# Kernel optimization log

Measured on AMD Instinct MI355X. Metric: run time of the kernel, lower is better.

Reference implementation:

```python
import jax, jax.numpy as jnp
import numpy as np

DIM = 256
HEADS = 8
DIM_HEAD = 32
INNER = HEADS * DIM_HEAD  # 256
SCALE = DIM_HEAD ** -0.5
NEG = -100.0

MASK0 = jnp.array([[0., 0., 0., NEG],
                   [0., 0., NEG, 0.],
                   [0., NEG, 0., 0.],
                   [NEG, 0., 0., 0.]], dtype=jnp.float32)
MASK1 = jnp.array([[0., NEG, 0., NEG],
                   [NEG, 0., NEG, 0.],
                   [NEG, NEG, NEG, NEG],
                   [NEG, NEG, NEG, NEG]], dtype=jnp.float32)


def setup_inputs() -> dict:
    key = jax.random.key(0)
    ks = jax.random.split(key, 8)
    b, p, d = 8, 3136, DIM
    return {
        "x": jax.random.normal(ks[0], (b, p, d), jnp.float32),
        "y": jax.random.normal(ks[1], (b, p, d), jnp.float32),
        "Wqkv_z": jax.random.normal(ks[2], (3 * INNER, d), jnp.float32) * 0.02,
        "Wout_z": jax.random.normal(ks[3], (d, INNER), jnp.float32) * 0.02,
        "bout_z": jnp.zeros((d,), jnp.float32),
        "Wqkv_z1": jax.random.normal(ks[4], (3 * INNER, d), jnp.float32) * 0.02,
        "Wout_z1": jax.random.normal(ks[5], (d, INNER), jnp.float32) * 0.02,
        "bout_z1": jnp.zeros((d,), jnp.float32),
    }


def _attn_stage(z, Wqkv, Wout, bout, mask):
    # z: [b, p, n=4, d]
    b, p, n, d = z.shape
    qkv = jnp.einsum('bpnd,ed->bpne', z, Wqkv)  # [b,p,4,3*inner]
    q, k, v = jnp.split(qkv, 3, axis=-1)
    def heads(t):  # [b,p,n,inner] -> [b,p,h,n,dh]
        return t.reshape(b, p, n, HEADS, DIM_HEAD).transpose(0, 1, 3, 2, 4)
    q, k, v = heads(q), heads(k), heads(v)
    dots = jnp.einsum('bphid,bphjd->bphij', q, k) * SCALE + mask
    attn = jax.nn.softmax(dots, axis=-1)
    out = jnp.einsum('bphij,bphjd->bphid', attn, v)
    out = out.transpose(0, 1, 3, 2, 4).reshape(b, p, n, INNER)
    return jnp.einsum('bpne,de->bpnd', out, Wout) + bout


def reference(x, y, Wqkv_z, Wout_z, bout_z, Wqkv_z1, Wout_z1, bout_z1):
    b, p, d = x.shape
    rgb_g = jnp.mean(x, axis=1, keepdims=True)    # avg_pool1d over p == mean
    dep_g = jnp.mean(y, axis=1, keepdims=True)
    rgb_g = jnp.broadcast_to(rgb_g, (b, p, d))
    dep_g = jnp.broadcast_to(dep_g, (b, p, d))
    z = jnp.stack([x, y, rgb_g, dep_g], axis=2)   # [b,p,4,d]
    z_out = _attn_stage(z, Wqkv_z, Wout_z, bout_z, MASK0)
    z_out1 = _attn_stage(z_out, Wqkv_z1, Wout_z1, bout_z1, MASK1)
    x1 = z_out1[:, :, 0, :]
    y1 = z_out1[:, :, 1, :]
    return (x1, y1)
```

## Files before the change

### kernel.cpp

```cpp
#include <hip/hip_runtime.h>

typedef unsigned short u16;
typedef unsigned int   u32;
typedef short bf16x8 __attribute__((ext_vector_type(8)));
typedef float f32x16 __attribute__((ext_vector_type(16)));

#define NB    8
#define NP    3136
#define DIM   256
#define PTILE 16
#define NEGM  (-100.0f)
#define QKSCALE 0.17677669529663687f

#define LDS_SZ  65536
#define Q0B     16384
#define K0B     32768
#define P0B     49152
#define Q1B     49152
#define P1B     32768
#define AO1LB   16384

__device__ __forceinline__ float bflo(u32 w) { return __uint_as_float(w << 16); }
__device__ __forceinline__ float bfhi(u32 w) { return __uint_as_float(w & 0xffff0000u); }

__device__ __forceinline__ u32 cvt_pk(float a, float b) {
  u32 r;
  asm("v_cvt_pk_bf16_f32 %0, %1, %2" : "=v"(r) : "v"(a), "v"(b));
  return r;
}

__device__ __forceinline__ void phase_fence() { __builtin_amdgcn_sched_barrier(0); }

template<int MASKI>
__device__ __forceinline__ float maskv(int i, int j) {
  if (MASKI == 0) return ((i ^ j) == 3) ? NEGM : 0.f;
  return (i >= 2 || ((i ^ j) & 1)) ? NEGM : 0.f;
}

#define FRAG(nt, ks) ((((size_t)(nt) * 16 + (ks)) * 64 + lane) * 8)

__device__ __forceinline__ void pack4(const float* __restrict__ W,
                                      u16* __restrict__ hi, u16* __restrict__ lo,
                                      int is_qkv, int pair0, int tid) {
  const int p    = pair0 + (tid >> 6);
  const int lane = tid & 63;
  const int nt = p >> 4, ks = p & 15;
  const int n  = nt * 32 + (lane & 31);
  const int k0 = ks * 16 + ((lane >> 5) << 3);
  const float scale = (is_qkv && n < 256) ? QKSCALE : 1.0f;
  const float* src = W + (size_t)n * 256 + k0;
  const size_t o = (((size_t)nt * 16 + ks) * 64 + lane) * 8;
#pragma unroll
  for (int j = 0; j < 8; j++) {
    float v = src[j] * scale;
    u32 wh = cvt_pk(v, v);
    hi[o + j] = (u16)wh;
    if (lo) lo[o + j] = (u16)cvt_pk(v - bflo(wh), 0.f);
  }
}

__global__ __launch_bounds__(256)
void prep1(const float* __restrict__ x, const float* __restrict__ y,
           float* __restrict__ part,
           const float* __restrict__ wqkv0, u16* __restrict__ wq0_hi,
           const float* __restrict__ wout1, u16* __restrict__ wo1_hi, u16* __restrict__ wo1_lo,
           const float* __restrict__ wqkv1, const float* __restrict__ wout0,
           float* __restrict__ Wc,
           const float* __restrict__ bout0, float* __restrict__ bq) {
  __shared__ float srow[256];
  const int bid = blockIdx.x;
  const int tid = threadIdx.x;
  if (bid < 1568) {
    const int ab = bid / 98;
    const int chunk = bid - ab * 98;
    const int b = ab & 7;
    const float* src = (ab >> 3) ? y : x;
    float s = 0.f;
    const int p0 = chunk * 32;
#pragma unroll 4
    for (int i = 0; i < 32; i++)
      s += src[((size_t)b * NP + p0 + i) * DIM + tid];
    part[((size_t)ab * 98 + chunk) * DIM + tid] = s;
  } else if (bid < 1664) {
    pack4(wqkv0, wq0_hi, nullptr, 1, (bid - 1568) * 4, tid);
  } else if (bid < 1696) {
    pack4(wout1, wo1_hi, wo1_lo, 0, (bid - 1664) * 4, tid);
  } else if (bid < 2464) {
    const int n = bid - 1696;
    srow[tid] = wqkv1[(size_t)n * 256 + tid];
    __syncthreads();
    float acc = 0.f;
#pragma unroll 8
    for (int d = 0; d < 256; d++)
      acc += srow[d] * wout0[(size_t)d * 256 + tid];
    Wc[(size_t)n * 256 + tid] = acc;
  } else {
    const int n = (bid - 2464) * 256 + tid;
    float s = 0.f;
    for (int d = 0; d < 256; d += 4) {
      const float4 w = *(const float4*)(wqkv1 + (size_t)n * 256 + d);
      const float4 bv = *(const float4*)(bout0 + d);
      s += w.x * bv.x + w.y * bv.y + w.z * bv.z + w.w * bv.w;
    }
    bq[n] = (n < 256) ? s * QKSCALE : s;
  }
}

__global__ __launch_bounds__(256)
void prep2(const float* __restrict__ part, const float* __restrict__ wqkv0,
           float* __restrict__ qkvg,
           const float* __restrict__ Wc, u16* __restrict__ wc_hi, u16* __restrict__ wc_lo) {
  __shared__ float srow[256];
  const int bid = blockIdx.x;
  const int tid = threadIdx.x;
  if (bid < 16) {
    float s = 0.f;
    for (int c = 0; c < 98; c++) s += part[((size_t)bid * 98 + c) * DIM + tid];
    srow[tid] = s * (1.0f / 3136.0f);
    __syncthreads();
    const int bt = (bid < 8) ? (2 * bid) : (2 * (bid - 8) + 1);
#pragma unroll
    for (int sct = 0; sct < 3; sct++) {
      const int e = sct * 256 + tid;
      float acc = 0.f;
      for (int d = 0; d < 256; d += 4) {
        const float4 w = *(const float4*)(wqkv0 + (size_t)e * 256 + d);
        acc += w.x * srow[d] + w.y * srow[d + 1] + w.z * srow[d + 2] + w.w * srow[d + 3];
      }
      qkvg[(size_t)bt * 768 + e] = (e < 256) ? acc * QKSCALE : acc;
    }
  } else {
    pack4(Wc, wc_hi, wc_lo, 1, (bid - 16) * 4, tid);
  }
}

__global__ __launch_bounds__(512, 4)
void fused_kernel(const float* __restrict__ x, const float* __restrict__ y,
                  const float* __restrict__ qkvg, float* __restrict__ outp,
                  const u16* __restrict__ wq0_hi,
                  const u16* __restrict__ wc_hi,  const u16* __restrict__ wc_lo,
                  const u16* __restrict__ wo1_hi, const u16* __restrict__ wo1_lo,
                  const float* __restrict__ bq,   const float* __restrict__ bout1) {
  extern __shared__ char lds[];
  const int tid  = threadIdx.x;
  const int lane = tid & 63;
  const int wave = tid >> 6;
  const int cl   = lane & 31;
  const int rh5  = lane >> 5;
  const int kgrp = rh5 << 3;
  const int b    = blockIdx.y;
  const int pos0 = blockIdx.x * PTILE;
  const int apos = wave * 2 + rh5;
  const int ah   = (lane >> 2) & 7;
  const int adq  = lane & 3;
  const float* qg = qkvg + (size_t)(b * 2) * 768;

  {
    const int r   = tid >> 4;
    const int cb  = (tid & 15) * 16;
    const int pos = pos0 + (r >> 1);
    const float* src = ((r & 1) ? y : x) + ((size_t)b * NP + pos) * DIM;
#pragma unroll
    for (int u = 0; u < 4; u++) {
      const int col = cb + u * 4;
      float4 v = *(const float4*)(src + col);
      uint2 hw;
      hw.x = cvt_pk(v.x, v.y);
      hw.y = cvt_pk(v.z, v.w);
      *(uint2*)(lds + ((r * 512 + col * 2) ^ ((r & 15) << 4))) = hw;
    }
  }
  __syncthreads();
  phase_fence();

  f32x16 av;
  {
    f32x16 aq, ak;
#pragma unroll
    for (int i = 0; i < 16; i++) { aq[i] = 0.f; ak[i] = 0.f; av[i] = 0.f; }
#pragma unroll 2
    for (int ks = 0; ks < 16; ks++) {
      const int k0 = ks * 16 + kgrp;
      bf16x8 ahf = *(const bf16x8*)(lds + ((cl * 512 + k0 * 2) ^ ((cl & 15) << 4)));
      bf16x8 bQ = *(const bf16x8*)(wq0_hi + FRAG(wave, ks));
      bf16x8 bK = *(const bf16x8*)(wq0_hi + FRAG(8 + wave, ks));
      bf16x8 bV = *(const bf16x8*)(wq0_hi + FRAG(16 + wave, ks));
      __builtin_amdgcn_s_setprio(1);
      aq = __builtin_amdgcn_mfma_f32_32x32x16_bf16(ahf, bQ, aq, 0, 0, 0);
      ak = __builtin_amdgcn_mfma_f32_32x32x16_bf16(ahf, bK, ak, 0, 0, 0);
      av = __builtin_amdgcn_mfma_f32_32x32x16_bf16(ahf, bV, av, 0, 0, 0);
      __builtin_amdgcn_s_setprio(0);
    }
    const int sw0 = ((cl ^ wave) & 7) << 3;
    const int bQd = Q0B + wave * 2048 + cl * 64;
    const int bKd = K0B + wave * 2048 + cl * 64;
#pragma unroll
    for (int gq = 0; gq < 4; gq++) {
      const int p20 = 8 * gq + 4 * rh5;
      uint2 wv;
      wv.x = cvt_pk(aq[4 * gq + 0], aq[4 * gq + 1]);
      wv.y = cvt_pk(aq[4 * gq + 2], aq[4 * gq + 3]);
      *(uint2*)(lds + bQd + ((p20 * 2) ^ sw0)) = wv;
      wv.x = cvt_pk(ak[4 * gq + 0], ak[4 * gq + 1]);
      wv.y = cvt_pk(ak[4 * gq + 2], ak[4 * gq + 3]);
      *(uint2*)(lds + bKd + ((p20 * 2) ^ sw0)) = wv;
    }
  }
  __syncthreads();
  phase_fence();

  {
    const int e0 = ah * 32 + adq * 8;
    float dots[4][4];
#pragma unroll
    for (int i = 0; i < 4; i++)
#pragma unroll
      for (int j = 0; j < 4; j++) dots[i][j] = 0.f;
#pragma unroll 2
    for (int dd = 0; dd < 8; dd++) {
      const int d = adq * 8 + dd;
      const int sw = ((d ^ ah) & 7) << 3;
      u32 qw = *(const u32*)(lds + Q0B + ah * 2048 + d * 64 + ((apos * 4) ^ sw));
      u32 kw = *(const u32*)(lds + K0B + ah * 2048 + d * 64 + ((apos * 4) ^ sw));
      float q[4] = { bflo(qw), bfhi(qw), qg[e0 + dd], qg[768 + e0 + dd] };
      float k[4] = { bflo(kw), bfhi(kw), qg[256 + e0 + dd], qg[1024 + e0 + dd] };
#pragma unroll
      for (int i = 0; i < 4; i++)
#pragma unroll
        for (int j = 0; j < 4; j++) dots[i][j] += q[i] * k[j];
    }
#pragma unroll
    for (int i = 0; i < 4; i++)
#pragma unroll
      for (int j = 0; j < 4; j++) {
        float s = dots[i][j];
        s += __shfl_xor(s, 1);
        s += __shfl_xor(s, 2);
        dots[i][j] = s + maskv<0>(i, j);
      }
    if (adq == 0) {
#pragma unroll
      for (int i = 0; i < 4; i++) {
        const float mx = fmaxf(fmaxf(dots[i][0], dots[i][1]), fmaxf(dots[i][2], dots[i][3]));
        const float e0_ = __expf(dots[i][0] - mx), e1_ = __expf(dots[i][1] - mx);
        const float e2_ = __expf(dots[i][2] - mx), e3_ = __expf(dots[i][3] - mx);
        const float inv = 1.f / (e0_ + e1_ + e2_ + e3_);
        float4 pv_ = { e0_ * inv, e1_ * inv, e2_ * inv, e3_ * inv };
        *(float4*)(lds + P0B + ((apos * 8 + ah) * 4 + i) * 16) = pv_;
      }
    }
  }
  __syncthreads();
  phase_fence();

  {
    const float vg2 = qg[512 + wave * 32 + cl];
    const float vg3 = qg[768 + 512 + wave * 32 + cl];
    const int c = wave * 32 + cl;
#pragma unroll
    for (int gq = 0; gq < 4; gq++) {
#pragma unroll
      for (int pp = 0; pp < 2; pp++) {
        const int pos = 4 * gq + 2 * rh5 + pp;
        const float v0 = av[4 * gq + 2 * pp], v1 = av[4 * gq + 2 * pp + 1];
#pragma unroll
        for (int i = 0; i < 4; i++) {
          float4 pi = *(const float4*)(lds + P0B + ((pos * 8 + wave) * 4 + i) * 16);
          const float o = pi.x * v0 + pi.y * v1 + pi.z * vg2 + pi.w * vg3;
          const int R = pos * 4 + i;
          *(u16*)(lds + ((R * 512 + c * 2) ^ ((R & 15) << 4))) = (u16)cvt_pk(o, o);
        }
      }
    }
  }
  __syncthreads();
  phase_fence();

  {
    f32x16 aq0, aq1;
#pragma unroll
    for (int i = 0; i < 16; i++) { aq0[i] = 0.f; aq1[i] = 0.f; }
#pragma unroll 1
    for (int ks = 0; ks < 16; ks++) {
      const int k0 = ks * 16 + kgrp;
      bf16x8 ah0 = *(const bf16x8*)(lds + ((cl * 512 + k0 * 2) ^ ((cl & 15) << 4)));
      bf16x8 ah1 = *(const bf16x8*)(lds + (((32 + cl) * 512 + k0 * 2) ^ (((32 + cl) & 15) << 4)));
      bf16x8 bh = *(const bf16x8*)(wc_hi + FRAG(wave, ks));
      bf16x8 bl = *(const bf16x8*)(wc_lo + FRAG(wave, ks));
      __builtin_amdgcn_s_setprio(1);
      aq0 = __builtin_amdgcn_mfma_f32_32x32x16_bf16(ah0, bh, aq0, 0, 0, 0);
      aq0 = __builtin_amdgcn_mfma_f32_32x32x16_bf16(ah0, bl, aq0, 0, 0, 0);
      aq1 = __builtin_amdgcn_mfma_f32_32x32x16_bf16(ah1, bh, aq1, 0, 0, 0);
      aq1 = __builtin_amdgcn_mfma_f32_32x32x16_bf16(ah1, bl, aq1, 0, 0, 0);
      __builtin_amdgcn_s_setprio(0);
    }
    const float qb = bq[wave * 32 + cl];
    const int swq = ((cl ^ wave) & 7) << 3;
    const int bQ1 = Q1B + wave * 2048 + cl * 64;
#pragma unroll
    for (int gq = 0; gq < 4; gq++) {
      const int posA = 2 * gq + rh5;
      *(u32*)(lds + bQ1 + ((posA * 4) ^ swq)) =
          cvt_pk(aq0[4 * gq] + qb, aq0[4 * gq + 1] + qb);
      *(u32*)(lds + bQ1 + (((posA + 8) * 4) ^ swq)) =
          cvt_pk(aq1[4 * gq] + qb, aq1[4 * gq + 1] + qb);
    }
  }
  phase_fence();
  uint2 kp0[4], kp1[4];
  {
    f32x16 ak0, ak1;
#pragma unroll
    for (int i = 0; i < 16; i++) { ak0[i] = 0.f; ak1[i] = 0.f; }
#pragma unroll 1
    for (int ks = 0; ks < 16; ks++) {
      const int k0 = ks * 16 + kgrp;
      bf16x8 ah0 = *(const bf16x8*)(lds + ((cl * 512 + k0 * 2) ^ ((cl & 15) << 4)));
      bf16x8 ah1 = *(const bf16x8*)(lds + (((32 + cl) * 512 + k0 * 2) ^ (((32 + cl) & 15) << 4)));
      bf16x8 bh = *(const bf16x8*)(wc_hi + FRAG(8 + wave, ks));
      bf16x8 bl = *(const bf16x8*)(wc_lo + FRAG(8 + wave, ks));
      __builtin_amdgcn_s_setprio(1);
      ak0 = __builtin_amdgcn_mfma_f32_32x32x16_bf16(ah0, bh, ak0, 0, 0, 0);
      ak0 = __builtin_amdgcn_mfma_f32_32x32x16_bf16(ah0, bl, ak0, 0, 0, 0);
      ak1 = __builtin_amdgcn_mfma_f32_32x32x16_bf16(ah1, bh, ak1, 0, 0, 0);
      ak1 = __builtin_amdgcn_mfma_f32_32x32x16_bf16(ah1, bl, ak1, 0, 0, 0);
      __builtin_amdgcn_s_setprio(0);
    }
    const float kb = bq[256 + wave * 32 + cl];
#pragma unroll
    for (int gq = 0; gq < 4; gq++) {
      kp0[gq].x = cvt_pk(ak0[4 * gq + 0] + kb, ak0[4 * gq + 1] + kb);
      kp0[gq].y = cvt_pk(ak0[4 * gq + 2] + kb, ak0[4 * gq + 3] + kb);
      kp1[gq].x = cvt_pk(ak1[4 * gq + 0] + kb, ak1[4 * gq + 1] + kb);
      kp1[gq].y = cvt_pk(ak1[4 * gq + 2] + kb, ak1[4 * gq + 3] + kb);
    }
  }
  phase_fence();
  f32x16 av0, av1;
  {
#pragma unroll
    for (int i = 0; i < 16; i++) { av0[i] = 0.f; av1[i] = 0.f; }
#pragma unroll 1
    for (int ks = 0; ks < 16; ks++) {
      const int k0 = ks * 16 + kgrp;
      bf16x8 ah0 = *(const bf16x8*)(lds + ((cl * 512 + k0 * 2) ^ ((cl & 15) << 4)));
      bf16x8 ah1 = *(const bf16x8*)(lds + (((32 + cl) * 512 + k0 * 2) ^ (((32 + cl) & 15) << 4)));
      bf16x8 bh = *(const bf16x8*)(wc_hi + FRAG(16 + wave, ks));
      bf16x8 bl = *(const bf16x8*)(wc_lo + FRAG(16 + wave, ks));
      __builtin_amdgcn_s_setprio(1);
      av0 = __builtin_amdgcn_mfma_f32_32x32x16_bf16(ah0, bh, av0, 0, 0, 0);
      av0 = __builtin_amdgcn_mfma_f32_32x32x16_bf16(ah0, bl, av0, 0, 0, 0);
      av1 = __builtin_amdgcn_mfma_f32_32x32x16_bf16(ah1, bh, av1, 0, 0, 0);
      av1 = __builtin_amdgcn_mfma_f32_32x32x16_bf16(ah1, bl, av1, 0, 0, 0);
      __builtin_amdgcn_s_setprio(0);
    }
    const float vb = bq[512 + wave * 32 + cl];
#pragma unroll
    for (int i = 0; i < 16; i++) { av0[i] += vb; av1[i] += vb; }
  }
  __syncthreads();
  phase_fence();

  {
    const int swk = ((cl ^ wave) & 7) << 4;
    const int bK1 = wave * 4096 + cl * 128;
#pragma unroll
    for (int gq = 0; gq < 4; gq++) {
      const int R0a = 8 * gq + 4 * rh5;
      *(uint2*)(lds + bK1 + ((R0a * 2) ^ swk)) = kp0[gq];
      *(uint2*)(lds + bK1 + (((R0a + 32) * 2) ^ swk)) = kp1[gq];
    }
  }
  __syncthreads();
  phase_fence();

  {
    float dots[2][4];
#pragma unroll
    for (int i = 0; i < 2; i++)
#pragma unroll
      for (int j = 0; j < 4; j++) dots[i][j] = 0.f;
#pragma unroll 2
    for (int dd = 0; dd < 8; dd++) {
      const int d = adq * 8 + dd;
      u32 qw = *(const u32*)(lds + Q1B + ah * 2048 + d * 64 +
                             ((apos * 4) ^ (((d ^ ah) & 7) << 3)));
      uint2 kw = *(const uint2*)(lds + ah * 4096 + d * 128 +
                                 ((apos * 8) ^ (((d ^ ah) & 7) << 4)));
      float q[2] = { bflo(qw), bfhi(qw) };
      float k[4] = { bflo(kw.x), bfhi(kw.x), bflo(kw.y), bfhi(kw.y) };
#pragma unroll
      for (int i = 0; i < 2; i++)
#pragma unroll
        for (int j = 0; j < 4; j++) dots[i][j] += q[i] * k[j];
    }
#pragma unroll
    for (int i = 0; i < 2; i++)
#pragma unroll
      for (int j = 0; j < 4; j++) {
        float s = dots[i][j];
        s += __shfl_xor(s, 1);
        s += __shfl_xor(s, 2);
        dots[i][j] = s + maskv<1>(i, j);
      }
    if (adq == 0) {
#pragma unroll
      for (int i = 0; i < 2; i++) {
        const float mx = fmaxf(fmaxf(dots[i][0], dots[i][1]), fmaxf(dots[i][2], dots[i][3]));
        const float e0_ = __expf(dots[i][0] - mx), e1_ = __expf(dots[i][1] - mx);
        const float e2_ = __expf(dots[i][2] - mx), e3_ = __expf(dots[i][3] - mx);
        const float inv = 1.f / (e0_ + e1_ + e2_ + e3_);
        float4 pv_ = { e0_ * inv, e1_ * inv, e2_ * inv, e3_ * inv };
        *(float4*)(lds + P1B + ((apos * 8 + ah) * 2 + i) * 16) = pv_;
      }
    }
  }
  __syncthreads();
  phase_fence();

  {
    const int c = wave * 32 + cl;
#pragma unroll
    for (int gq = 0; gq < 4; gq++) {
      const int posA = 2 * gq + rh5;
#pragma unroll
      for (int i = 0; i < 2; i++) {
        float4 pa = *(const float4*)(lds + P1B + ((posA * 8 + wave) * 2 + i) * 16);
        const float o0 = pa.x * av0[4 * gq] + pa.y * av0[4 * gq + 1] +
                         pa.z * av0[4 * gq + 2] + pa.w * av0[4 * gq + 3];
        const int r0 = posA * 2 + i;
        const u32 h0 = cvt_pk(o0, o0);
        const int bo0 = (r0 * 512 + c * 2) ^ ((r0 & 15) << 4);
        *(u16*)(lds + bo0) = (u16)h0;
        *(u16*)(lds + AO1LB + bo0) = (u16)cvt_pk(o0 - bflo(h0), 0.f);
        float4 pb = *(const float4*)(lds + P1B + (((posA + 8) * 8 + wave) * 2 + i) * 16);
        const float o1 = pb.x * av1[4 * gq] + pb.y * av1[4 * gq + 1] +
                         pb.z * av1[4 * gq + 2] + pb.w * av1[4 * gq + 3];
        const int r1 = (posA + 8) * 2 + i;
        const u32 h1 = cvt_pk(o1, o1);
        const int bo1 = (r1 * 512 + c * 2) ^ ((r1 & 15) << 4);
        *(u16*)(lds + bo1) = (u16)h1;
        *(u16*)(lds + AO1LB + bo1) = (u16)cvt_pk(o1 - bflo(h1), 0.f);
      }
    }
  }
  __syncthreads();
  phase_fence();

  {
    f32x16 acc2;
#pragma unroll
    for (int i = 0; i < 16; i++) acc2[i] = 0.f;
#pragma unroll 2
    for (int ks = 0; ks < 16; ks++) {
      const int k0 = ks * 16 + kgrp;
      const int bo = (cl * 512 + k0 * 2) ^ ((cl & 15) << 4);
      bf16x8 ahf = *(const bf16x8*)(lds + bo);
      bf16x8 alf = *(const bf16x8*)(lds + AO1LB + bo);
      bf16x8 bh = *(const bf16x8*)(wo1_hi + FRAG(wave, ks));
      bf16x8 bl = *(const bf16x8*)(wo1_lo + FRAG(wave, ks));
      __builtin_amdgcn_s_setprio(1);
      acc2 = __builtin_amdgcn_mfma_f32_32x32x16_bf16(ahf, bh, acc2, 0, 0, 0);
      acc2 = __builtin_amdgcn_mfma_f32_32x32x16_bf16(ahf, bl, acc2, 0, 0, 0);
      acc2 = __builtin_amdgcn_mfma_f32_32x32x16_bf16(alf, bh, acc2, 0, 0, 0);
      __builtin_amdgcn_s_setprio(0);
    }
    const int c = wave * 32 + cl;
    const float bc = bout1[c];
    const size_t TOT = (size_t)NB * NP * DIM;
#pragma unroll
    for (int i = 0; i < 16; i++) {
      const int r = (i & 3) + ((i >> 2) << 3) + 4 * rh5;
      const int pos = pos0 + (r >> 1);
      const float v = acc2[i] + bc;
      if ((r & 1) == 0) outp[((size_t)b * NP + pos) * DIM + c] = v;
      else              outp[TOT + ((size_t)b * NP + pos) * DIM + c] = v;
    }
  }
}

extern "C" void kernel_launch(void* const* d_in, const int* in_sizes, int n_in,
                              void* d_out, int out_size, void* d_ws, size_t ws_size,
                              hipStream_t stream) {
  const float* x     = (const float*)d_in[0];
  const float* y     = (const float*)d_in[1];
  const float* wqkv0 = (const float*)d_in[2];
  const float* wout0 = (const float*)d_in[3];
  const float* bout0 = (const float*)d_in[4];
  const float* wqkv1 = (const float*)d_in[5];
  const float* wout1 = (const float*)d_in[6];
  const float* bout1 = (const float*)d_in[7];

  float* part = (float*)d_ws;
  float* Wc   = part + (size_t)16 * 98 * DIM;
  float* bq   = Wc + (size_t)768 * 256;
  float* qkvg = bq + 768;
  u16* w = (u16*)(qkvg + (size_t)8 * 2 * 768);
  u16* wq0_hi = w; w += (size_t)768 * 256;
  u16* wc_hi  = w; w += (size_t)768 * 256;
  u16* wc_lo  = w; w += (size_t)768 * 256;
  u16* wo1_hi = w; w += (size_t)256 * 256;
  u16* wo1_lo = w; w += (size_t)256 * 256;

  prep1<<<dim3(2467), dim3(256), 0, stream>>>(
      x, y, part, wqkv0, wq0_hi, wout1, wo1_hi, wo1_lo,
      wqkv1, wout0, Wc, bout0, bq);
  prep2<<<dim3(112), dim3(256), 0, stream>>>(part, wqkv0, qkvg, Wc, wc_hi, wc_lo);

  fused_kernel<<<dim3(NP / PTILE, NB), dim3(512), LDS_SZ, stream>>>(
      x, y, qkvg, (float*)d_out,
      wq0_hi, wc_hi, wc_lo, wo1_hi, wo1_lo, bq, bout1);
}
```

Before: 221.8 us.

## Shrink fused-kernel LDS footprint and fold Wc packing into prep1

Remaps LDS regions in the fused kernel so the stage-0 softmax probabilities, the stage-1 Q, the bf16 activation tile and K1 reuse overlapping offsets, cutting dynamic LDS from 64KB to 52KB and raising the launch-bounds occupancy hint from 4 to 6 blocks. Separately, the Wqkv1·Wout0 combined-weight product is computed in 32-row tiles inside prep1 and packed directly into hi/lo bf16 fragments, removing the fp32 Wc intermediate and the packing blocks from prep2. The higher occupancy hint may force register spills, and the aliased LDS regions depend on barrier ordering being correct.

```diff
diff --git a/kernel.cpp b/kernel.cpp
--- a/kernel.cpp
+++ b/kernel.cpp
@@ -12,12 +12,12 @@
 #define NEGM  (-100.0f)
 #define QKSCALE 0.17677669529663687f
 
-#define LDS_SZ  65536
+#define LDS_SZ  53248
 #define Q0B     16384
 #define K0B     32768
-#define P0B     49152
-#define Q1B     49152
-#define P1B     32768
+#define A1B     16384
+#define K1B     16384
+#define P1B     49152
 #define AO1LB   16384
 
 __device__ __forceinline__ float bflo(u32 w) { return __uint_as_float(w << 16); }
@@ -65,9 +65,9 @@
            const float* __restrict__ wqkv0, u16* __restrict__ wq0_hi,
            const float* __restrict__ wout1, u16* __restrict__ wo1_hi, u16* __restrict__ wo1_lo,
            const float* __restrict__ wqkv1, const float* __restrict__ wout0,
-           float* __restrict__ Wc,
+           u16* __restrict__ wc_hi, u16* __restrict__ wc_lo,
            const float* __restrict__ bout0, float* __restrict__ bq) {
-  __shared__ float srow[256];
+  __shared__ float smem[32 * 256];
   const int bid = blockIdx.x;
   const int tid = threadIdx.x;
   if (bid < 1568) {
@@ -85,17 +85,42 @@
     pack4(wqkv0, wq0_hi, nullptr, 1, (bid - 1568) * 4, tid);
   } else if (bid < 1696) {
     pack4(wout1, wo1_hi, wo1_lo, 0, (bid - 1664) * 4, tid);
-  } else if (bid < 2464) {
-    const int n = bid - 1696;
-    srow[tid] = wqkv1[(size_t)n * 256 + tid];
+  } else if (bid < 1720) {
+    const int nt = bid - 1696;
+#pragma unroll 4
+    for (int r = 0; r < 32; r++)
+      smem[r * 256 + tid] = wqkv1[(size_t)(nt * 32 + r) * 256 + tid];
     __syncthreads();
-    float acc = 0.f;
-#pragma unroll 8
-    for (int d = 0; d < 256; d++)
-      acc += srow[d] * wout0[(size_t)d * 256 + tid];
-    Wc[(size_t)n * 256 + tid] = acc;
+    float acc[32];
+#pragma unroll
+    for (int n = 0; n < 32; n++) acc[n] = 0.f;
+    for (int d = 0; d < 256; d++) {
+      const float w0 = wout0[(size_t)d * 256 + tid];
+#pragma unroll
+      for (int n = 0; n < 32; n++) acc[n] += smem[n * 256 + d] * w0;
+    }
+    __syncthreads();
+    const float scale = (nt < 8) ? QKSCALE : 1.0f;
+#pragma unroll
+    for (int n = 0; n < 32; n++) smem[n * 256 + tid] = acc[n] * scale;
+    __syncthreads();
+    const int lane = tid & 63;
+#pragma unroll 1
+    for (int pass = 0; pass < 4; pass++) {
+      const int ks = pass * 4 + (tid >> 6);
+      const int nl = lane & 31;
+      const int k0 = ks * 16 + ((lane >> 5) << 3);
+      const size_t o = (((size_t)nt * 16 + ks) * 64 + lane) * 8;
+#pragma unroll
+      for (int j = 0; j < 8; j++) {
+        float v = smem[nl * 256 + k0 + j];
+        u32 wh = cvt_pk(v, v);
+        wc_hi[o + j] = (u16)wh;
+        wc_lo[o + j] = (u16)cvt_pk(v - bflo(wh), 0.f);
+      }
+    }
   } else {
-    const int n = (bid - 2464) * 256 + tid;
+    const int n = (bid - 1720) * 256 + tid;
     float s = 0.f;
     for (int d = 0; d < 256; d += 4) {
       const float4 w = *(const float4*)(wqkv1 + (size_t)n * 256 + d);
@@ -108,33 +133,28 @@
 
 __global__ __launch_bounds__(256)
 void prep2(const float* __restrict__ part, const float* __restrict__ wqkv0,
-           float* __restrict__ qkvg,
-           const float* __restrict__ Wc, u16* __restrict__ wc_hi, u16* __restrict__ wc_lo) {
+           float* __restrict__ qkvg) {
   __shared__ float srow[256];
   const int bid = blockIdx.x;
   const int tid = threadIdx.x;
-  if (bid < 16) {
-    float s = 0.f;
-    for (int c = 0; c < 98; c++) s += part[((size_t)bid * 98 + c) * DIM + tid];
-    srow[tid] = s * (1.0f / 3136.0f);
-    __syncthreads();
-    const int bt = (bid < 8) ? (2 * bid) : (2 * (bid - 8) + 1);
-#pragma unroll
-    for (int sct = 0; sct < 3; sct++) {
-      const int e = sct * 256 + tid;
-      float acc = 0.f;
-      for (int d = 0; d < 256; d += 4) {
-        const float4 w = *(const float4*)(wqkv0 + (size_t)e * 256 + d);
-        acc += w.x * srow[d] + w.y * srow[d + 1] + w.z * srow[d + 2] + w.w * srow[d + 3];
-      }
-      qkvg[(size_t)bt * 768 + e] = (e < 256) ? acc * QKSCALE : acc;
-    }
-  } else {
-    pack4(Wc, wc_hi, wc_lo, 1, (bid - 16) * 4, tid);
-  }
-}
-
-__global__ __launch_bounds__(512, 4)
+  float s = 0.f;
+  for (int c = 0; c < 98; c++) s += part[((size_t)bid * 98 + c) * DIM + tid];
+  srow[tid] = s * (1.0f / 3136.0f);
+  __syncthreads();
+  const int bt = (bid < 8) ? (2 * bid) : (2 * (bid - 8) + 1);
+#pragma unroll
+  for (int sct = 0; sct < 3; sct++) {
+    const int e = sct * 256 + tid;
+    float acc = 0.f;
+    for (int d = 0; d < 256; d += 4) {
+      const float4 w = *(const float4*)(wqkv0 + (size_t)e * 256 + d);
+      acc += w.x * srow[d] + w.y * srow[d + 1] + w.z * srow[d + 2] + w.w * srow[d + 3];
+    }
+    qkvg[(size_t)bt * 768 + e] = (e < 256) ? acc * QKSCALE : acc;
+  }
+}
+
+__global__ __launch_bounds__(512, 6)
 void fused_kernel(const float* __restrict__ x, const float* __restrict__ y,
                   const float* __restrict__ qkvg, float* __restrict__ outp,
                   const u16* __restrict__ wq0_hi,
@@ -246,7 +266,7 @@
         const float e2_ = __expf(dots[i][2] - mx), e3_ = __expf(dots[i][3] - mx);
         const float inv = 1.f / (e0_ + e1_ + e2_ + e3_);
         float4 pv_ = { e0_ * inv, e1_ * inv, e2_ * inv, e3_ * inv };
-        *(float4*)(lds + P0B + ((apos * 8 + ah) * 4 + i) * 16) = pv_;
+        *(float4*)(lds + ((apos * 8 + ah) * 4 + i) * 16) = pv_;
       }
     }
   }
@@ -265,10 +285,10 @@
         const float v0 = av[4 * gq + 2 * pp], v1 = av[4 * gq + 2 * pp + 1];
 #pragma unroll
         for (int i = 0; i < 4; i++) {
-          float4 pi = *(const float4*)(lds + P0B + ((pos * 8 + wave) * 4 + i) * 16);
+          float4 pi = *(const float4*)(lds + ((pos * 8 + wave) * 4 + i) * 16);
           const float o = pi.x * v0 + pi.y * v1 + pi.z * vg2 + pi.w * vg3;
           const int R = pos * 4 + i;
-          *(u16*)(lds + ((R * 512 + c * 2) ^ ((R & 15) << 4))) = (u16)cvt_pk(o, o);
+          *(u16*)(lds + A1B + ((R * 512 + c * 2) ^ ((R & 15) << 4))) = (u16)cvt_pk(o, o);
         }
       }
     }
@@ -283,8 +303,8 @@
 #pragma unroll 1
     for (int ks = 0; ks < 16; ks++) {
       const int k0 = ks * 16 + kgrp;
-      bf16x8 ah0 = *(const bf16x8*)(lds + ((cl * 512 + k0 * 2) ^ ((cl & 15) << 4)));
-      bf16x8 ah1 = *(const bf16x8*)(lds + (((32 + cl) * 512 + k0 * 2) ^ (((32 + cl) & 15) << 4)));
+      bf16x8 ah0 = *(const bf16x8*)(lds + A1B + ((cl * 512 + k0 * 2) ^ ((cl & 15) << 4)));
+      bf16x8 ah1 = *(const bf16x8*)(lds + A1B + (((32 + cl) * 512 + k0 * 2) ^ (((32 + cl) & 15) << 4)));
       bf16x8 bh = *(const bf16x8*)(wc_hi + FRAG(wave, ks));
       bf16x8 bl = *(const bf16x8*)(wc_lo + FRAG(wave, ks));
       __builtin_amdgcn_s_setprio(1);
@@ -296,7 +316,7 @@
     }
     const float qb = bq[wave * 32 + cl];
     const int swq = ((cl ^ wave) & 7) << 3;
-    const int bQ1 = Q1B + wave * 2048 + cl * 64;
+    const int bQ1 = wave * 2048 + cl * 64;
 #pragma unroll
     for (int gq = 0; gq < 4; gq++) {
       const int posA = 2 * gq + rh5;
@@ -315,8 +335,8 @@
 #pragma unroll 1
     for (int ks = 0; ks < 16; ks++) {
       const int k0 = ks * 16 + kgrp;
-      bf16x8 ah0 = *(const bf16x8*)(lds + ((cl * 512 + k0 * 2) ^ ((cl & 15) << 4)));
-      bf16x8 ah1 = *(const bf16x8*)(lds + (((32 + cl) * 512 + k0 * 2) ^ (((32 + cl) & 15) << 4)));
+      bf16x8 ah0 = *(const bf16x8*)(lds + A1B + ((cl * 512 + k0 * 2) ^ ((cl & 15) << 4)));
+      bf16x8 ah1 = *(const bf16x8*)(lds + A1B + (((32 + cl) * 512 + k0 * 2) ^ (((32 + cl) & 15) << 4)));
       bf16x8 bh = *(const bf16x8*)(wc_hi + FRAG(8 + wave, ks));
       bf16x8 bl = *(const bf16x8*)(wc_lo + FRAG(8 + wave, ks));
       __builtin_amdgcn_s_setprio(1);
@@ -343,8 +363,8 @@
 #pragma unroll 1
     for (int ks = 0; ks < 16; ks++) {
       const int k0 = ks * 16 + kgrp;
-      bf16x8 ah0 = *(const bf16x8*)(lds + ((cl * 512 + k0 * 2) ^ ((cl & 15) << 4)));
-      bf16x8 ah1 = *(const bf16x8*)(lds + (((32 + cl) * 512 + k0 * 2) ^ (((32 + cl) & 15) << 4)));
+      bf16x8 ah0 = *(const bf16x8*)(lds + A1B + ((cl * 512 + k0 * 2) ^ ((cl & 15) << 4)));
+      bf16x8 ah1 = *(const bf16x8*)(lds + A1B + (((32 + cl) * 512 + k0 * 2) ^ (((32 + cl) & 15) << 4)));
       bf16x8 bh = *(const bf16x8*)(wc_hi + FRAG(16 + wave, ks));
       bf16x8 bl = *(const bf16x8*)(wc_lo + FRAG(16 + wave, ks));
       __builtin_amdgcn_s_setprio(1);
@@ -363,7 +383,7 @@
 
   {
     const int swk = ((cl ^ wave) & 7) << 4;
-    const int bK1 = wave * 4096 + cl * 128;
+    const int bK1 = K1B + wave * 4096 + cl * 128;
 #pragma unroll
     for (int gq = 0; gq < 4; gq++) {
       const int R0a = 8 * gq + 4 * rh5;
@@ -383,9 +403,9 @@
 #pragma unroll 2
     for (int dd = 0; dd < 8; dd++) {
       const int d = adq * 8 + dd;
-      u32 qw = *(const u32*)(lds + Q1B + ah * 2048 + d * 64 +
+      u32 qw = *(const u32*)(lds + ah * 2048 + d * 64 +
                              ((apos * 4) ^ (((d ^ ah) & 7) << 3)));
-      uint2 kw = *(const uint2*)(lds + ah * 4096 + d * 128 +
+      uint2 kw = *(const uint2*)(lds + K1B + ah * 4096 + d * 128 +
                                  ((apos * 8) ^ (((d ^ ah) & 7) << 4)));
       float q[2] = { bflo(qw), bfhi(qw) };
       float k[4] = { bflo(kw.x), bfhi(kw.x), bflo(kw.y), bfhi(kw.y) };
@@ -492,8 +512,7 @@
   const float* bout1 = (const float*)d_in[7];
 
   float* part = (float*)d_ws;
-  float* Wc   = part + (size_t)16 * 98 * DIM;
-  float* bq   = Wc + (size_t)768 * 256;
+  float* bq   = part + (size_t)16 * 98 * DIM;
   float* qkvg = bq + 768;
   u16* w = (u16*)(qkvg + (size_t)8 * 2 * 768);
   u16* wq0_hi = w; w += (size_t)768 * 256;
@@ -502,10 +521,10 @@
   u16* wo1_hi = w; w += (size_t)256 * 256;
   u16* wo1_lo = w; w += (size_t)256 * 256;
 
-  prep1<<<dim3(2467), dim3(256), 0, stream>>>(
+  prep1<<<dim3(1723), dim3(256), 0, stream>>>(
       x, y, part, wqkv0, wq0_hi, wout1, wo1_hi, wo1_lo,
-      wqkv1, wout0, Wc, bout0, bq);
-  prep2<<<dim3(112), dim3(256), 0, stream>>>(part, wqkv0, qkvg, Wc, wc_hi, wc_lo);
+      wqkv1, wout0, wc_hi, wc_lo, bout0, bq);
+  prep2<<<dim3(16), dim3(256), 0, stream>>>(part, wqkv0, qkvg);
 
   fused_kernel<<<dim3(NP / PTILE, NB), dim3(512), LDS_SZ, stream>>>(
       x, y, qkvg, (float*)d_out,
```

Measured after the change: 280.4 us. 26.4% more time.

## Shrink LDS footprint and pack V to bf16 to raise occupancy

Applied to the files above, without the earlier changes.

Rearranges the LDS buffer map (P0 at offset 0, stage-1 activations at A1B, K1 overlapping, P1 moved) so the block needs 52 KB instead of 64 KB of shared memory. Stage-1 V accumulators are packed into bf16 registers instead of being kept as two fp32 16-wide vectors. Launch bounds move from 4 to 6 blocks per CU minimum. The aim is more resident waves to hide latency. The cost is that V is rounded to bf16 before the attention-weighted sum, which adds precision loss, and the tighter register budget may cause spills.

```diff
diff --git a/kernel.cpp b/kernel.cpp
--- a/kernel.cpp
+++ b/kernel.cpp
@@ -12,12 +12,12 @@
 #define NEGM  (-100.0f)
 #define QKSCALE 0.17677669529663687f
 
-#define LDS_SZ  65536
+#define LDS_SZ  53248
 #define Q0B     16384
 #define K0B     32768
-#define P0B     49152
-#define Q1B     49152
-#define P1B     32768
+#define A1B     16384
+#define K1B     16384
+#define P1B     49152
 #define AO1LB   16384
 
 __device__ __forceinline__ float bflo(u32 w) { return __uint_as_float(w << 16); }
@@ -134,7 +134,7 @@
   }
 }
 
-__global__ __launch_bounds__(512, 4)
+__global__ __launch_bounds__(512, 6)
 void fused_kernel(const float* __restrict__ x, const float* __restrict__ y,
                   const float* __restrict__ qkvg, float* __restrict__ outp,
                   const u16* __restrict__ wq0_hi,
@@ -246,7 +246,7 @@
         const float e2_ = __expf(dots[i][2] - mx), e3_ = __expf(dots[i][3] - mx);
         const float inv = 1.f / (e0_ + e1_ + e2_ + e3_);
         float4 pv_ = { e0_ * inv, e1_ * inv, e2_ * inv, e3_ * inv };
-        *(float4*)(lds + P0B + ((apos * 8 + ah) * 4 + i) * 16) = pv_;
+        *(float4*)(lds + ((apos * 8 + ah) * 4 + i) * 16) = pv_;
       }
     }
   }
@@ -265,10 +265,10 @@
         const float v0 = av[4 * gq + 2 * pp], v1 = av[4 * gq + 2 * pp + 1];
 #pragma unroll
         for (int i = 0; i < 4; i++) {
-          float4 pi = *(const float4*)(lds + P0B + ((pos * 8 + wave) * 4 + i) * 16);
+          float4 pi = *(const float4*)(lds + ((pos * 8 + wave) * 4 + i) * 16);
           const float o = pi.x * v0 + pi.y * v1 + pi.z * vg2 + pi.w * vg3;
           const int R = pos * 4 + i;
-          *(u16*)(lds + ((R * 512 + c * 2) ^ ((R & 15) << 4))) = (u16)cvt_pk(o, o);
+          *(u16*)(lds + A1B + ((R * 512 + c * 2) ^ ((R & 15) << 4))) = (u16)cvt_pk(o, o);
         }
       }
     }
@@ -283,8 +283,8 @@
 #pragma unroll 1
     for (int ks = 0; ks < 16; ks++) {
       const int k0 = ks * 16 + kgrp;
-      bf16x8 ah0 = *(const bf16x8*)(lds + ((cl * 512 + k0 * 2) ^ ((cl & 15) << 4)));
-      bf16x8 ah1 = *(const bf16x8*)(lds + (((32 + cl) * 512 + k0 * 2) ^ (((32 + cl) & 15) << 4)));
+      bf16x8 ah0 = *(const bf16x8*)(lds + A1B + ((cl * 512 + k0 * 2) ^ ((cl & 15) << 4)));
+      bf16x8 ah1 = *(const bf16x8*)(lds + A1B + (((32 + cl) * 512 + k0 * 2) ^ (((32 + cl) & 15) << 4)));
       bf16x8 bh = *(const bf16x8*)(wc_hi + FRAG(wave, ks));
       bf16x8 bl = *(const bf16x8*)(wc_lo + FRAG(wave, ks));
       __builtin_amdgcn_s_setprio(1);
@@ -296,7 +296,7 @@
     }
     const float qb = bq[wave * 32 + cl];
     const int swq = ((cl ^ wave) & 7) << 3;
-    const int bQ1 = Q1B + wave * 2048 + cl * 64;
+    const int bQ1 = wave * 2048 + cl * 64;
 #pragma unroll
     for (int gq = 0; gq < 4; gq++) {
       const int posA = 2 * gq + rh5;
@@ -315,8 +315,8 @@
 #pragma unroll 1
     for (int ks = 0; ks < 16; ks++) {
       const int k0 = ks * 16 + kgrp;
-      bf16x8 ah0 = *(const bf16x8*)(lds + ((cl * 512 + k0 * 2) ^ ((cl & 15) << 4)));
-      bf16x8 ah1 = *(const bf16x8*)(lds + (((32 + cl) * 512 + k0 * 2) ^ (((32 + cl) & 15) << 4)));
+      bf16x8 ah0 = *(const bf16x8*)(lds + A1B + ((cl * 512 + k0 * 2) ^ ((cl & 15) << 4)));
+      bf16x8 ah1 = *(const bf16x8*)(lds + A1B + (((32 + cl) * 512 + k0 * 2) ^ (((32 + cl) & 15) << 4)));
       bf16x8 bh = *(const bf16x8*)(wc_hi + FRAG(8 + wave, ks));
       bf16x8 bl = *(const bf16x8*)(wc_lo + FRAG(8 + wave, ks));
       __builtin_amdgcn_s_setprio(1);
@@ -336,15 +336,16 @@
     }
   }
   phase_fence();
-  f32x16 av0, av1;
-  {
+  uint2 avp0[4], avp1[4];
+  {
+    f32x16 av0, av1;
 #pragma unroll
     for (int i = 0; i < 16; i++) { av0[i] = 0.f; av1[i] = 0.f; }
 #pragma unroll 1
     for (int ks = 0; ks < 16; ks++) {
       const int k0 = ks * 16 + kgrp;
-      bf16x8 ah0 = *(const bf16x8*)(lds + ((cl * 512 + k0 * 2) ^ ((cl & 15) << 4)));
-      bf16x8 ah1 = *(const bf16x8*)(lds + (((32 + cl) * 512 + k0 * 2) ^ (((32 + cl) & 15) << 4)));
+      bf16x8 ah0 = *(const bf16x8*)(lds + A1B + ((cl * 512 + k0 * 2) ^ ((cl & 15) << 4)));
+      bf16x8 ah1 = *(const bf16x8*)(lds + A1B + (((32 + cl) * 512 + k0 * 2) ^ (((32 + cl) & 15) << 4)));
       bf16x8 bh = *(const bf16x8*)(wc_hi + FRAG(16 + wave, ks));
       bf16x8 bl = *(const bf16x8*)(wc_lo + FRAG(16 + wave, ks));
       __builtin_amdgcn_s_setprio(1);
@@ -356,14 +357,19 @@
     }
     const float vb = bq[512 + wave * 32 + cl];
 #pragma unroll
-    for (int i = 0; i < 16; i++) { av0[i] += vb; av1[i] += vb; }
+    for (int gq = 0; gq < 4; gq++) {
+      avp0[gq].x = cvt_pk(av0[4 * gq + 0] + vb, av0[4 * gq + 1] + vb);
+      avp0[gq].y = cvt_pk(av0[4 * gq + 2] + vb, av0[4 * gq + 3] + vb);
+      avp1[gq].x = cvt_pk(av1[4 * gq + 0] + vb, av1[4 * gq + 1] + vb);
+      avp1[gq].y = cvt_pk(av1[4 * gq + 2] + vb, av1[4 * gq + 3] + vb);
+    }
   }
   __syncthreads();
   phase_fence();
 
   {
     const int swk = ((cl ^ wave) & 7) << 4;
-    const int bK1 = wave * 4096 + cl * 128;
+    const int bK1 = K1B + wave * 4096 + cl * 128;
 #pragma unroll
     for (int gq = 0; gq < 4; gq++) {
       const int R0a = 8 * gq + 4 * rh5;
@@ -383,9 +389,9 @@
 #pragma unroll 2
     for (int dd = 0; dd < 8; dd++) {
       const int d = adq * 8 + dd;
-      u32 qw = *(const u32*)(lds + Q1B + ah * 2048 + d * 64 +
+      u32 qw = *(const u32*)(lds + ah * 2048 + d * 64 +
                              ((apos * 4) ^ (((d ^ ah) & 7) << 3)));
-      uint2 kw = *(const uint2*)(lds + ah * 4096 + d * 128 +
+      uint2 kw = *(const uint2*)(lds + K1B + ah * 4096 + d * 128 +
                                  ((apos * 8) ^ (((d ^ ah) & 7) << 4)));
       float q[2] = { bflo(qw), bfhi(qw) };
       float k[4] = { bflo(kw.x), bfhi(kw.x), bflo(kw.y), bfhi(kw.y) };
@@ -423,19 +429,21 @@
 #pragma unroll
     for (int gq = 0; gq < 4; gq++) {
       const int posA = 2 * gq + rh5;
+      const float a00 = bflo(avp0[gq].x), a01 = bfhi(avp0[gq].x);
+      const float a02 = bflo(avp0[gq].y), a03 = bfhi(avp0[gq].y);
+      const float a10 = bflo(avp1[gq].x), a11 = bfhi(avp1[gq].x);
+      const float a12 = bflo(avp1[gq].y), a13 = bfhi(avp1[gq].y);
 #pragma unroll
       for (int i = 0; i < 2; i++) {
         float4 pa = *(const float4*)(lds + P1B + ((posA * 8 + wave) * 2 + i) * 16);
-        const float o0 = pa.x * av0[4 * gq] + pa.y * av0[4 * gq + 1] +
-                         pa.z * av0[4 * gq + 2] + pa.w * av0[4 * gq + 3];
+        const float o0 = pa.x * a00 + pa.y * a01 + pa.z * a02 + pa.w * a03;
         const int r0 = posA * 2 + i;
         const u32 h0 = cvt_pk(o0, o0);
         const int bo0 = (r0 * 512 + c * 2) ^ ((r0 & 15) << 4);
         *(u16*)(lds + bo0) = (u16)h0;
         *(u16*)(lds + AO1LB + bo0) = (u16)cvt_pk(o0 - bflo(h0), 0.f);
         float4 pb = *(const float4*)(lds + P1B + (((posA + 8) * 8 + wave) * 2 + i) * 16);
-        const float o1 = pb.x * av1[4 * gq] + pb.y * av1[4 * gq + 1] +
-                         pb.z * av1[4 * gq + 2] + pb.w * av1[4 * gq + 3];
+        const float o1 = pb.x * a10 + pb.y * a11 + pb.z * a12 + pb.w * a13;
         const int r1 = (posA + 8) * 2 + i;
         const u32 h1 = cvt_pk(o1, o1);
         const int bo1 = (r1 * 512 + c * 2) ^ ((r1 & 15) << 4);
```

Measured after the change: 229.8 us. 3.6% more time.
